# Performance work log

Hardware: AMD Instinct MI355X
Metric: run time of the kernel (lower is better)

Reference implementation:

```python
import jax, jax.numpy as jnp
import numpy as np

LMBDA = 1000.0
GAMMA = 1.0  # resolvent_gamma


def setup_inputs() -> dict:
    key = jax.random.key(0)
    k = jax.random.split(key, 6)
    B, K, N, D = 16, 128, 8000, 256
    return {
        "evals_a": jax.random.uniform(k[0], (B, K), dtype=jnp.float32) + 1e-3,
        "pinv_a": jax.random.normal(k[1], (B, K, N), dtype=jnp.float32),
        "descr_a": jax.random.normal(k[2], (B, D, N), dtype=jnp.float32),
        "evals_b": jax.random.uniform(k[3], (B, K), dtype=jnp.float32) + 1e-3,
        "pinv_b": jax.random.normal(k[4], (B, K, N), dtype=jnp.float32),
        "descr_b": jax.random.normal(k[5], (B, D, N), dtype=jnp.float32),
    }


def _compute_mask(evals_a, evals_b, gamma):
    # evals_*: [B, K]. Per-batch normalization by joint max, then resolvent mask.
    scale = jnp.maximum(evals_a.max(axis=-1), evals_b.max(axis=-1))[:, None]
    ga = jnp.power(evals_a / scale, gamma)[:, None, :]  # [B, 1, K]
    gb = jnp.power(evals_b / scale, gamma)[:, :, None]  # [B, K, 1]
    M_re = gb / (gb * gb + 1.0) - ga / (ga * ga + 1.0)
    M_im = 1.0 / (gb * gb + 1.0) - 1.0 / (ga * ga + 1.0)
    return M_re * M_re + M_im * M_im  # [B, K, K]


def _compute_fmap(sdescr_a, sdescr_b, mask, lmbda):
    # sdescr_*: [B, D, K]; mask: [B, K, K]
    AA_aa = jnp.einsum("bdk,bdl->bkl", sdescr_a, sdescr_a)  # [B, K, K]
    AA_ba = jnp.einsum("bdk,bdl->bkl", sdescr_b, sdescr_a)  # [B, K, K]
    K = mask.shape[-1]
    eye = jnp.eye(K, dtype=mask.dtype)
    # Per row i: (AA_aa + lmbda * diag(mask[b, i, :]))^{-1} AA_ba[b, i, :]^T
    A = AA_aa[:, None, :, :] + lmbda * mask[..., None] * eye  # [B, K, K, K]
    Cab = jnp.linalg.solve(A, AA_ba[..., None])[..., 0]  # [B, K, K], row i = solution
    return Cab


def reference(evals_a, pinv_a, descr_a, evals_b, pinv_b, descr_b):
    # spectral descriptor projection: (pinv @ descr^T)^T -> [B, D, K]
    sdescr_a = jnp.einsum("bkn,bdn->bdk", pinv_a, descr_a)
    sdescr_b = jnp.einsum("bkn,bdn->bdk", pinv_b, descr_b)
    mask_ab = _compute_mask(evals_a, evals_b, GAMMA)
    fmap_12 = _compute_fmap(sdescr_a, sdescr_b, mask_ab, LMBDA)
    mask_ba = _compute_mask(evals_b, evals_a, GAMMA)
    fmap_21 = _compute_fmap(sdescr_b, sdescr_a, mask_ba, LMBDA)
    return (fmap_12, fmap_21)
```

## Files before the change

### kernel.cpp

```cpp
#include <hip/hip_runtime.h>

#define BB 16
#define KD 128
#define ND 8000
#define DD 256
#define LMB 1000.0f

typedef __attribute__((ext_vector_type(8))) short bf16x8;
typedef __attribute__((ext_vector_type(4))) short bf16x4;
typedef __attribute__((ext_vector_type(4))) float f32x4;
typedef unsigned short ushort_t;

__device__ __forceinline__ void split_bf16(float x, ushort_t& h, ushort_t& l) {
    unsigned int bi = __float_as_uint(x);
    h = (ushort_t)(bi >> 16);
    float lo = x - __uint_as_float(bi & 0xFFFF0000u);
    l = (ushort_t)(__float_as_uint(lo) >> 16);
}

__device__ __forceinline__ void split_bf16_rne(float x, ushort_t& h, ushort_t& l) {
    unsigned int bi = __float_as_uint(x);
    h = (ushort_t)(bi >> 16);
    float lo = x - __uint_as_float(bi & 0xFFFF0000u);
    unsigned int lb = __float_as_uint(lo);
    lb = lb + 0x7FFFu + ((lb >> 16) & 1u);
    l = (ushort_t)(lb >> 16);
}

__device__ __forceinline__ void cvt8(f32x4 a, f32x4 b, bf16x8& h, bf16x8& l) {
    #pragma unroll
    for (int j = 0; j < 4; ++j) {
        ushort_t hh, ll;
        split_bf16(a[j], hh, ll); h[j] = (short)hh; l[j] = (short)ll;
        split_bf16(b[j], hh, ll); h[4 + j] = (short)hh; l[4 + j] = (short)ll;
    }
}

__device__ __forceinline__ void gll16(const float* g, float* l) {
    __builtin_amdgcn_global_load_lds(
        (const __attribute__((address_space(1))) void*)g,
        (__attribute__((address_space(3))) void*)l, 16, 0, 0);
}

#define ROWS 384
#define CHF 32
#define NSL 8
#define SBUF_FL 12288
#define DEPTH 3

__global__ __attribute__((amdgpu_flat_work_group_size(1024, 1024)))
void proj_kernel(
    const float* __restrict__ pinv_a, const float* __restrict__ descr_a,
    const float* __restrict__ pinv_b, const float* __restrict__ descr_b,
    float* __restrict__ sd_a, float* __restrict__ sd_b)
{
    const int b = blockIdx.x, which = blockIdx.y, s = blockIdx.z;
    const float* P  = (which ? pinv_b  : pinv_a)  + (size_t)b * KD * ND;
    const float* Dm = (which ? descr_b : descr_a) + (size_t)b * DD * ND;
    float* outp = (which ? sd_b : sd_a) + (size_t)b * KD * DD;

    __shared__ float Sbuf[DEPTH][SBUF_FL];

    const int tid = threadIdx.x;
    const int lane = tid & 63;
    const int wid = tid >> 6;
    const int wm = wid >> 2, wn = wid & 3;
    const int fr = lane & 15;
    const int kg = lane >> 4;
    const int NC = (s < 2) ? 32 : 31;

    const float* gp[3];
    int lof[3];
    #pragma unroll
    for (int u = 0; u < 3; ++u) {
        int I = wid * 3 + u;
        int r = I * 8 + (lane >> 3);
        int c4 = (lane & 7) ^ (r & 7);
        const float* rowp = (r < KD) ? (P + (size_t)r * ND) : (Dm + (size_t)(r - KD) * ND);
        gp[u] = rowp + c4 * 4;
        lof[u] = I * 256;
    }

    f32x4 acc[2][4];
    #pragma unroll
    for (int i = 0; i < 2; ++i)
        #pragma unroll
        for (int j = 0; j < 4; ++j) acc[i][j] = (f32x4){0.f, 0.f, 0.f, 0.f};

    #pragma unroll
    for (int u = 0; u < 3; ++u) gll16(gp[u] + s * CHF, &Sbuf[0][lof[u]]);
    #pragma unroll
    for (int u = 0; u < 3; ++u) gll16(gp[u] + (s + NSL) * CHF, &Sbuf[1][lof[u]]);

    for (int t = 0; t < NC; ++t) {
        if (t + 1 < NC) {
            asm volatile("s_waitcnt vmcnt(3)" ::: "memory");
        } else {
            asm volatile("s_waitcnt vmcnt(0)" ::: "memory");
        }
        __builtin_amdgcn_sched_barrier(0);
        __builtin_amdgcn_s_barrier();
        __builtin_amdgcn_sched_barrier(0);
        if (t + 2 < NC) {
            const int noff = (s + NSL * (t + 2)) * CHF;
            float* dst = &Sbuf[(t + 2) % DEPTH][0];
            #pragma unroll
            for (int u = 0; u < 3; ++u) gll16(gp[u] + noff, dst + lof[u]);
        }
        __builtin_amdgcn_sched_barrier(0);

        const float* base = &Sbuf[t % DEPTH][0];

        bf16x8 Ah[2], Al[2];
        #pragma unroll
        for (int mi = 0; mi < 2; ++mi) {
            const int rA = wm * 32 + mi * 16 + fr;
            const int ra7 = rA & 7;
            f32x4 a0 = *(const f32x4*)(base + rA * CHF + (((2 * kg)     ^ ra7) << 2));
            f32x4 a1 = *(const f32x4*)(base + rA * CHF + (((2 * kg + 1) ^ ra7) << 2));
            cvt8(a0, a1, Ah[mi], Al[mi]);
        }
        #pragma unroll
        for (int ni = 0; ni < 4; ++ni) {
            const int rB = KD + wn * 64 + ni * 16 + fr;
            const int rb7 = rB & 7;
            f32x4 b0 = *(const f32x4*)(base + rB * CHF + (((2 * kg)     ^ rb7) << 2));
            f32x4 b1 = *(const f32x4*)(base + rB * CHF + (((2 * kg + 1) ^ rb7) << 2));
            bf16x8 Bh, Bl;
            cvt8(b0, b1, Bh, Bl);
            #pragma unroll
            for (int mi = 0; mi < 2; ++mi) {
                acc[mi][ni] = __builtin_amdgcn_mfma_f32_16x16x32_bf16(Ah[mi], Bh, acc[mi][ni], 0, 0, 0);
                acc[mi][ni] = __builtin_amdgcn_mfma_f32_16x16x32_bf16(Ah[mi], Bl, acc[mi][ni], 0, 0, 0);
                acc[mi][ni] = __builtin_amdgcn_mfma_f32_16x16x32_bf16(Al[mi], Bh, acc[mi][ni], 0, 0, 0);
            }
        }
        __builtin_amdgcn_sched_barrier(0);
    }

    #pragma unroll
    for (int mi = 0; mi < 2; ++mi)
        #pragma unroll
        for (int ni = 0; ni < 4; ++ni) {
            int rbase = wm * 32 + mi * 16 + kg * 4;
            int ccol  = wn * 64 + ni * 16 + fr;
            #pragma unroll
            for (int r = 0; r < 4; ++r)
                atomicAdd(&outp[(size_t)(rbase + r) * DD + ccol], acc[mi][ni][r]);
        }
}

#define GSTR 68
__global__ __launch_bounds__(512, 2) void gram_kernel(
    const float* __restrict__ sd_a, const float* __restrict__ sd_b,
    float* __restrict__ AA)
{
    const int b = blockIdx.x, m = blockIdx.y, dchunk = blockIdx.z;
    const float* X = (m == 0) ? sd_a : sd_b;
    const float* Y = (m == 2) ? sd_a : X;
    X += (size_t)b * KD * DD;
    Y += (size_t)b * KD * DD;
    float* outp = AA + ((size_t)m * BB + b) * KD * KD;
    const int d0 = dchunk * 64;

    __shared__ ushort_t Xh[KD][GSTR], Xl[KD][GSTR];
    __shared__ ushort_t Yh[KD][GSTR], Yl[KD][GSTR];

    const int tid = threadIdx.x;
    const int lane = tid & 63;
    const int wid = tid >> 6;
    const int wm = wid >> 2, wn = wid & 3;
    const int fr = lane & 15;
    const int kg = lane >> 4;

    f32x4 acc[4][2];
    #pragma unroll
    for (int i = 0; i < 4; ++i)
        #pragma unroll
        for (int j = 0; j < 2; ++j) acc[i][j] = (f32x4){0.f, 0.f, 0.f, 0.f};

    #pragma unroll
    for (int u = 0; u < 8; ++u) {
        int idx = tid + (u & 3) * 512;
        int r = idx >> 4, c4 = idx & 15;
        const float* src = (u < 4) ? X : Y;
        float4 v = *(const float4*)(src + (size_t)r * DD + d0 + c4 * 4);
        float xs[4] = {v.x, v.y, v.z, v.w};
        bf16x4 hv, lv;
        #pragma unroll
        for (int q = 0; q < 4; ++q) {
            ushort_t hh, ll;
            split_bf16_rne(xs[q], hh, ll);
            hv[q] = (short)hh; lv[q] = (short)ll;
        }
        if (u < 4) {
            *(bf16x4*)&Xh[r][c4 * 4] = hv;
            *(bf16x4*)&Xl[r][c4 * 4] = lv;
        } else {
            *(bf16x4*)&Yh[r][c4 * 4] = hv;
            *(bf16x4*)&Yl[r][c4 * 4] = lv;
        }
    }
    __syncthreads();

    #pragma unroll
    for (int kk = 0; kk < 2; ++kk) {
        const int co = kk * 32 + kg * 8;
        bf16x8 Ah[4], Al[4];
        #pragma unroll
        for (int mi = 0; mi < 4; ++mi) {
            int r = wm * 64 + mi * 16 + fr;
            Ah[mi] = *(const bf16x8*)&Xh[r][co];
            Al[mi] = *(const bf16x8*)&Xl[r][co];
        }
        #pragma unroll
        for (int ni = 0; ni < 2; ++ni) {
            int c = wn * 32 + ni * 16 + fr;
            bf16x8 Bh = *(const bf16x8*)&Yh[c][co];
            bf16x8 Bl = *(const bf16x8*)&Yl[c][co];
            #pragma unroll
            for (int mi = 0; mi < 4; ++mi) {
                acc[mi][ni] = __builtin_amdgcn_mfma_f32_16x16x32_bf16(Ah[mi], Bh, acc[mi][ni], 0, 0, 0);
                acc[mi][ni] = __builtin_amdgcn_mfma_f32_16x16x32_bf16(Ah[mi], Bl, acc[mi][ni], 0, 0, 0);
                acc[mi][ni] = __builtin_amdgcn_mfma_f32_16x16x32_bf16(Al[mi], Bh, acc[mi][ni], 0, 0, 0);
            }
        }
    }

    #pragma unroll
    for (int mi = 0; mi < 4; ++mi)
        #pragma unroll
        for (int ni = 0; ni < 2; ++ni) {
            int rbase = wm * 64 + mi * 16 + kg * 4;
            int ccol  = wn * 32 + ni * 16 + fr;
            #pragma unroll
            for (int rr = 0; rr < 4; ++rr)
                atomicAdd(&outp[(size_t)(rbase + rr) * KD + ccol], acc[mi][ni][rr]);
        }
}

__global__ __launch_bounds__(512, 2) void invert_kernel(
    const float* __restrict__ AA, ushort_t* __restrict__ Hbf)
{
    const int b = blockIdx.x, which = blockIdx.y;
    const float* src = AA + ((size_t)which * BB + b) * KD * KD;
    ushort_t* dh = Hbf + (size_t)(which * BB + b) * 2 * KD * KD;
    ushort_t* dl = dh + (size_t)KD * KD;

    __shared__ float rowbuf[2][KD];
    __shared__ float colbuf[2][KD];

    const int tid = threadIdx.x;
    const int rb = tid >> 5;
    const int cg = tid & 31;

    f32x4 Areg[8];
    #pragma unroll
    for (int r = 0; r < 8; ++r)
        Areg[r] = *(const f32x4*)(src + (size_t)(rb * 8 + r) * KD + cg * 4);

    if (rb == 0) *(f32x4*)&rowbuf[0][cg * 4] = Areg[0];
    if (cg == 0) {
        #pragma unroll
        for (int r = 0; r < 8; ++r) colbuf[0][rb * 8 + r] = Areg[r].x;
    }
    __syncthreads();

    for (int j = 0; j < KD; ++j) {
        const int cur = j & 1, nxt = cur ^ 1;
        const int jrb = j >> 3, jr = j & 7, jcg = j >> 2, jc = j & 3;
        const float pv = 1.0f / rowbuf[cur][j];
        const f32x4 orow = *(const f32x4*)&rowbuf[cur][cg * 4];
        const f32x4 prow = orow * pv;
        const bool mycg = (cg == jcg);
        const bool myrb = (rb == jrb);

        #pragma unroll
        for (int r = 0; r < 8; ++r) {
            const float cm = colbuf[cur][rb * 8 + r];
            const float cmul = -cm * pv;
            const bool piv = myrb && (r == jr);
            f32x4 nv;
            nv.x = piv ? prow.x : fmaf(cmul, orow.x, Areg[r].x);
            nv.y = piv ? prow.y : fmaf(cmul, orow.y, Areg[r].y);
            nv.z = piv ? prow.z : fmaf(cmul, orow.z, Areg[r].z);
            nv.w = piv ? prow.w : fmaf(cmul, orow.w, Areg[r].w);
            if (mycg) {
                const float fixv = piv ? pv : cmul;
                nv.x = (jc == 0) ? fixv : nv.x;
                nv.y = (jc == 1) ? fixv : nv.y;
                nv.z = (jc == 2) ? fixv : nv.z;
                nv.w = (jc == 3) ? fixv : nv.w;
            }
            Areg[r] = nv;
        }

        if (j + 1 < KD) {
            const int njrb = (j + 1) >> 3, njr = (j + 1) & 7;
            const int njcg = (j + 1) >> 2, njc = (j + 1) & 3;
            if (rb == njrb) {
                #pragma unroll
                for (int r = 0; r < 8; ++r)
                    if (r == njr) *(f32x4*)&rowbuf[nxt][cg * 4] = Areg[r];
            }
            if (cg == njcg) {
                #pragma unroll
                for (int r = 0; r < 8; ++r) {
                    const f32x4 a = Areg[r];
                    const float e = (njc == 0) ? a.x : (njc == 1) ? a.y : (njc == 2) ? a.z : a.w;
                    colbuf[nxt][rb * 8 + r] = e;
                }
            }
        }
        __syncthreads();
    }

    #pragma unroll
    for (int r = 0; r < 8; ++r) {
        bf16x4 hv, lv;
        #pragma unroll
        for (int q = 0; q < 4; ++q) {
            ushort_t hh, ll;
            split_bf16(Areg[r][q], hh, ll);
            hv[q] = (short)hh; lv[q] = (short)ll;
        }
        const size_t off = (size_t)(rb * 8 + r) * KD + cg * 4;
        *(bf16x4*)(dh + off) = hv;
        *(bf16x4*)(dl + off) = lv;
    }
}

#define NTERMS 3
#define HSTR 136
__global__ __launch_bounds__(512) void solve_kernel(
    const float* __restrict__ AAba, const float* __restrict__ ea_g,
    const float* __restrict__ eb_g, const ushort_t* __restrict__ Hbf,
    float* __restrict__ outp)
{
    const int b = blockIdx.x, cg = blockIdx.y, which = blockIdx.z;
    const ushort_t* Hg = Hbf + (size_t)(which * BB + b) * 2 * KD * KD;
    const float* Rs = AAba + (size_t)b * KD * KD;
    float* op = outp + ((size_t)which * BB + b) * KD * KD;
    const int i0 = cg * 32;

    __shared__ ushort_t Hh[KD][HSTR], Hl[KD][HSTR];
    __shared__ ushort_t Wh[32][HSTR], Wl[32][HSTR];
    __shared__ float lmT[KD][33];
    __shared__ float tC[KD], uC[KD], tR[32], uR[32];
    __shared__ float red[256];

    const int tid = threadIdx.x;
    const int lane = tid & 63;
    const int wid = tid >> 6;
    const int wl = wid & 3, wi = wid >> 2;
    const int fr = lane & 15;
    const int kg = lane >> 4;

    if (tid < 256) {
        float e = (tid < KD) ? ea_g[b * KD + tid] : eb_g[b * KD + (tid - KD)];
        red[tid] = e;
    }
    __syncthreads();
    for (int s = 128; s > 0; s >>= 1) {
        if (tid < s) red[tid] = fmaxf(red[tid], red[tid + s]);
        __syncthreads();
    }
    const float is = 1.0f / red[0];
    const float* Ce = which ? eb_g : ea_g;
    const float* Re = which ? ea_g : eb_g;
    if (tid < KD) {
        float g = Ce[b * KD + tid] * is;
        float den = 1.0f / (g * g + 1.0f);
        tC[tid] = g * den; uC[tid] = den;
    } else if (tid < KD + 32) {
        int i = tid - KD;
        float g = Re[b * KD + i0 + i] * is;
        float den = 1.0f / (g * g + 1.0f);
        tR[i] = g * den; uR[i] = den;
    }
    __syncthreads();
    #pragma unroll
    for (int u = 0; u < 8; ++u) {
        int idx = tid + u * 512;
        int l = idx >> 5, i = idx & 31;
        float re = tR[i] - tC[l], im = uR[i] - uC[l];
        lmT[l][i] = LMB * (re * re + im * im);
    }

    #pragma unroll
    for (int u = 0; u < 4; ++u) {
        int idx = tid + u * 512;
        int row = idx >> 4, g8 = idx & 15;
        *(bf16x8*)&Hh[row][g8 * 8] = *(const bf16x8*)(Hg + (size_t)row * KD + g8 * 8);
        *(bf16x8*)&Hl[row][g8 * 8] = *(const bf16x8*)(Hg + (size_t)KD * KD + (size_t)row * KD + g8 * 8);
    }
    if (which == 0) {
        #pragma unroll
        for (int u = 0; u < 2; ++u) {
            int idx4 = (tid + u * 512) * 4;
            int i = idx4 >> 7, d = idx4 & 127;
            f32x4 v = *(const f32x4*)(Rs + (size_t)(i0 + i) * KD + d);
            bf16x4 hv, lv;
            #pragma unroll
            for (int q = 0; q < 4; ++q) {
                ushort_t hh, ll;
                split_bf16(v[q], hh, ll);
                hv[q] = (short)hh; lv[q] = (short)ll;
            }
            *(bf16x4*)&Wh[i][d] = hv;
            *(bf16x4*)&Wl[i][d] = lv;
        }
    } else {
        #pragma unroll
        for (int u = 0; u < 8; ++u) {
            int idx = tid + u * 512;
            int i = idx & 31, d = idx >> 5;
            float v = Rs[(size_t)d * KD + i0 + i];
            ushort_t hh, ll;
            split_bf16(v, hh, ll);
            Wh[i][d] = hh; Wl[i][d] = ll;
        }
    }
    __syncthreads();

    f32x4 xacc[2];
    xacc[0] = (f32x4){0.f, 0.f, 0.f, 0.f};
    xacc[1] = (f32x4){0.f, 0.f, 0.f, 0.f};

    for (int t = 0; t < NTERMS; ++t) {
        f32x4 az[2];
        az[0] = (f32x4){0.f, 0.f, 0.f, 0.f};
        az[1] = (f32x4){0.f, 0.f, 0.f, 0.f};
        #pragma unroll
        for (int kk = 0; kk < 4; ++kk) {
            const int co = kk * 32 + kg * 8;
            bf16x8 Bh = *(const bf16x8*)&Wh[wi * 16 + fr][co];
            bf16x8 Bl = *(const bf16x8*)&Wl[wi * 16 + fr][co];
            #pragma unroll
            for (int mi = 0; mi < 2; ++mi) {
                const int rA = wl * 32 + mi * 16 + fr;
                bf16x8 Ah_ = *(const bf16x8*)&Hh[rA][co];
                bf16x8 Al_ = *(const bf16x8*)&Hl[rA][co];
                az[mi] = __builtin_amdgcn_mfma_f32_16x16x32_bf16(Ah_, Bh, az[mi], 0, 0, 0);
                az[mi] = __builtin_amdgcn_mfma_f32_16x16x32_bf16(Ah_, Bl, az[mi], 0, 0, 0);
                az[mi] = __builtin_amdgcn_mfma_f32_16x16x32_bf16(Al_, Bh, az[mi], 0, 0, 0);
            }
        }
        const float sg = (t & 1) ? -1.f : 1.f;
        #pragma unroll
        for (int mi = 0; mi < 2; ++mi) {
            xacc[mi][0] += sg * az[mi][0];
            xacc[mi][1] += sg * az[mi][1];
            xacc[mi][2] += sg * az[mi][2];
            xacc[mi][3] += sg * az[mi][3];
        }
        if (t + 1 < NTERMS) {
            __syncthreads();
            const int i = wi * 16 + fr;
            #pragma unroll
            for (int mi = 0; mi < 2; ++mi) {
                const int l0 = wl * 32 + mi * 16 + kg * 4;
                bf16x4 hv, lv;
                #pragma unroll
                for (int r = 0; r < 4; ++r) {
                    float w = lmT[l0 + r][i] * az[mi][r];
                    ushort_t hh, ll;
                    split_bf16(w, hh, ll);
                    hv[r] = (short)hh; lv[r] = (short)ll;
                }
                *(bf16x4*)&Wh[i][l0] = hv;
                *(bf16x4*)&Wl[i][l0] = lv;
            }
            __syncthreads();
        }
    }

    const int i = wi * 16 + fr;
    #pragma unroll
    for (int mi = 0; mi < 2; ++mi) {
        const int l0 = wl * 32 + mi * 16 + kg * 4;
        float4 o;
        o.x = xacc[mi][0]; o.y = xacc[mi][1]; o.z = xacc[mi][2]; o.w = xacc[mi][3];
        *(float4*)(op + (size_t)(i0 + i) * KD + l0) = o;
    }
}

extern "C" void kernel_launch(void* const* d_in, const int* in_sizes, int n_in,
                              void* d_out, int out_size, void* d_ws, size_t ws_size,
                              hipStream_t stream) {
    (void)in_sizes; (void)n_in; (void)out_size; (void)ws_size;
    const float* evals_a = (const float*)d_in[0];
    const float* pinv_a  = (const float*)d_in[1];
    const float* descr_a = (const float*)d_in[2];
    const float* evals_b = (const float*)d_in[3];
    const float* pinv_b  = (const float*)d_in[4];
    const float* descr_b = (const float*)d_in[5];
    float* out = (float*)d_out;
    float* ws = (float*)d_ws;

    const size_t SD = (size_t)BB * KD * DD;
    const size_t MM = (size_t)BB * KD * KD;
    float* sd_a  = ws;
    float* sd_b  = sd_a + SD;
    float* AA    = sd_b + SD;
    ushort_t* Hbf = (ushort_t*)(AA + 3 * MM);

    hipMemsetAsync(sd_a, 0, (2 * SD + 3 * MM) * sizeof(float), stream);
    proj_kernel<<<dim3(BB, 2, NSL), 1024, 0, stream>>>(pinv_a, descr_a, pinv_b, descr_b, sd_a, sd_b);
    gram_kernel<<<dim3(BB, 3, 4), 512, 0, stream>>>(sd_a, sd_b, AA);
    invert_kernel<<<dim3(BB, 2), 512, 0, stream>>>(AA, Hbf);
    solve_kernel<<<dim3(BB, 4, 2), 512, 0, stream>>>(AA + 2 * MM, evals_a, evals_b, Hbf, out);
}
```

Baseline: 258.4 us.

## Fuse matrix inversion and Neumann-series solve into one kernel

Merges invert_kernel and solve_kernel into a single invsolve_kernel. The inverted matrix is split into bf16 hi/lo parts and written straight into shared memory rather than round-tripped through global workspace. Each block then loops over all four 32-row column groups in sequence. This removes a kernel launch and the global write and read of the inverse. In exchange, parallelism for the solve phase drops from 128 blocks to 32 blocks on a large GPU.

```diff
diff --git a/kernel.cpp b/kernel.cpp
--- a/kernel.cpp
+++ b/kernel.cpp
@@ -239,16 +239,24 @@
         }
 }
 
-__global__ __launch_bounds__(512, 2) void invert_kernel(
-    const float* __restrict__ AA, ushort_t* __restrict__ Hbf)
+#define NTERMS 3
+#define HSTR 136
+__global__ __launch_bounds__(512) void invsolve_kernel(
+    const float* __restrict__ AA, const float* __restrict__ ea_g,
+    const float* __restrict__ eb_g, float* __restrict__ outp_)
 {
     const int b = blockIdx.x, which = blockIdx.y;
     const float* src = AA + ((size_t)which * BB + b) * KD * KD;
-    ushort_t* dh = Hbf + (size_t)(which * BB + b) * 2 * KD * KD;
-    ushort_t* dl = dh + (size_t)KD * KD;
+    const float* Rs  = AA + (size_t)2 * BB * KD * KD + (size_t)b * KD * KD;
+    float* op = outp_ + ((size_t)which * BB + b) * KD * KD;
 
     __shared__ float rowbuf[2][KD];
     __shared__ float colbuf[2][KD];
+    __shared__ ushort_t Hh[KD][HSTR], Hl[KD][HSTR];
+    __shared__ ushort_t Wh[32][HSTR], Wl[32][HSTR];
+    __shared__ float lmT[KD][33];
+    __shared__ float tC[KD], uC[KD], tR[32], uR[32];
+    __shared__ float red[256];
 
     const int tid = threadIdx.x;
     const int rb = tid >> 5;
@@ -317,45 +325,14 @@
 
     #pragma unroll
     for (int r = 0; r < 8; ++r) {
-        bf16x4 hv, lv;
         #pragma unroll
         for (int q = 0; q < 4; ++q) {
             ushort_t hh, ll;
             split_bf16(Areg[r][q], hh, ll);
-            hv[q] = (short)hh; lv[q] = (short)ll;
-        }
-        const size_t off = (size_t)(rb * 8 + r) * KD + cg * 4;
-        *(bf16x4*)(dh + off) = hv;
-        *(bf16x4*)(dl + off) = lv;
-    }
-}
-
-#define NTERMS 3
-#define HSTR 136
-__global__ __launch_bounds__(512) void solve_kernel(
-    const float* __restrict__ AAba, const float* __restrict__ ea_g,
-    const float* __restrict__ eb_g, const ushort_t* __restrict__ Hbf,
-    float* __restrict__ outp)
-{
-    const int b = blockIdx.x, cg = blockIdx.y, which = blockIdx.z;
-    const ushort_t* Hg = Hbf + (size_t)(which * BB + b) * 2 * KD * KD;
-    const float* Rs = AAba + (size_t)b * KD * KD;
-    float* op = outp + ((size_t)which * BB + b) * KD * KD;
-    const int i0 = cg * 32;
-
-    __shared__ ushort_t Hh[KD][HSTR], Hl[KD][HSTR];
-    __shared__ ushort_t Wh[32][HSTR], Wl[32][HSTR];
-    __shared__ float lmT[KD][33];
-    __shared__ float tC[KD], uC[KD], tR[32], uR[32];
-    __shared__ float red[256];
-
-    const int tid = threadIdx.x;
-    const int lane = tid & 63;
-    const int wid = tid >> 6;
-    const int wl = wid & 3, wi = wid >> 2;
-    const int fr = lane & 15;
-    const int kg = lane >> 4;
-
+            Hh[rb * 8 + r][cg * 4 + q] = hh;
+            Hl[rb * 8 + r][cg * 4 + q] = ll;
+        }
+    }
     if (tid < 256) {
         float e = (tid < KD) ? ea_g[b * KD + tid] : eb_g[b * KD + (tid - KD)];
         red[tid] = e;
@@ -372,116 +349,120 @@
         float g = Ce[b * KD + tid] * is;
         float den = 1.0f / (g * g + 1.0f);
         tC[tid] = g * den; uC[tid] = den;
-    } else if (tid < KD + 32) {
-        int i = tid - KD;
-        float g = Re[b * KD + i0 + i] * is;
-        float den = 1.0f / (g * g + 1.0f);
-        tR[i] = g * den; uR[i] = den;
     }
     __syncthreads();
-    #pragma unroll
-    for (int u = 0; u < 8; ++u) {
-        int idx = tid + u * 512;
-        int l = idx >> 5, i = idx & 31;
-        float re = tR[i] - tC[l], im = uR[i] - uC[l];
-        lmT[l][i] = LMB * (re * re + im * im);
-    }
-
-    #pragma unroll
-    for (int u = 0; u < 4; ++u) {
-        int idx = tid + u * 512;
-        int row = idx >> 4, g8 = idx & 15;
-        *(bf16x8*)&Hh[row][g8 * 8] = *(const bf16x8*)(Hg + (size_t)row * KD + g8 * 8);
-        *(bf16x8*)&Hl[row][g8 * 8] = *(const bf16x8*)(Hg + (size_t)KD * KD + (size_t)row * KD + g8 * 8);
-    }
-    if (which == 0) {
-        #pragma unroll
-        for (int u = 0; u < 2; ++u) {
-            int idx4 = (tid + u * 512) * 4;
-            int i = idx4 >> 7, d = idx4 & 127;
-            f32x4 v = *(const f32x4*)(Rs + (size_t)(i0 + i) * KD + d);
-            bf16x4 hv, lv;
-            #pragma unroll
-            for (int q = 0; q < 4; ++q) {
-                ushort_t hh, ll;
-                split_bf16(v[q], hh, ll);
-                hv[q] = (short)hh; lv[q] = (short)ll;
-            }
-            *(bf16x4*)&Wh[i][d] = hv;
-            *(bf16x4*)&Wl[i][d] = lv;
-        }
-    } else {
+
+    const int lane = tid & 63;
+    const int wid = tid >> 6;
+    const int wl = wid & 3, wi = wid >> 2;
+    const int fr = lane & 15;
+    const int kg = lane >> 4;
+
+    for (int cgi = 0; cgi < 4; ++cgi) {
+        const int i0 = cgi * 32;
+        __syncthreads();
+        if (tid < 32) {
+            float g = Re[b * KD + i0 + tid] * is;
+            float den = 1.0f / (g * g + 1.0f);
+            tR[tid] = g * den; uR[tid] = den;
+        }
+        __syncthreads();
         #pragma unroll
         for (int u = 0; u < 8; ++u) {
             int idx = tid + u * 512;
-            int i = idx & 31, d = idx >> 5;
-            float v = Rs[(size_t)d * KD + i0 + i];
-            ushort_t hh, ll;
-            split_bf16(v, hh, ll);
-            Wh[i][d] = hh; Wl[i][d] = ll;
-        }
-    }
-    __syncthreads();
-
-    f32x4 xacc[2];
-    xacc[0] = (f32x4){0.f, 0.f, 0.f, 0.f};
-    xacc[1] = (f32x4){0.f, 0.f, 0.f, 0.f};
-
-    for (int t = 0; t < NTERMS; ++t) {
-        f32x4 az[2];
-        az[0] = (f32x4){0.f, 0.f, 0.f, 0.f};
-        az[1] = (f32x4){0.f, 0.f, 0.f, 0.f};
-        #pragma unroll
-        for (int kk = 0; kk < 4; ++kk) {
-            const int co = kk * 32 + kg * 8;
-            bf16x8 Bh = *(const bf16x8*)&Wh[wi * 16 + fr][co];
-            bf16x8 Bl = *(const bf16x8*)&Wl[wi * 16 + fr][co];
-            #pragma unroll
-            for (int mi = 0; mi < 2; ++mi) {
-                const int rA = wl * 32 + mi * 16 + fr;
-                bf16x8 Ah_ = *(const bf16x8*)&Hh[rA][co];
-                bf16x8 Al_ = *(const bf16x8*)&Hl[rA][co];
-                az[mi] = __builtin_amdgcn_mfma_f32_16x16x32_bf16(Ah_, Bh, az[mi], 0, 0, 0);
-                az[mi] = __builtin_amdgcn_mfma_f32_16x16x32_bf16(Ah_, Bl, az[mi], 0, 0, 0);
-                az[mi] = __builtin_amdgcn_mfma_f32_16x16x32_bf16(Al_, Bh, az[mi], 0, 0, 0);
-            }
-        }
-        const float sg = (t & 1) ? -1.f : 1.f;
-        #pragma unroll
-        for (int mi = 0; mi < 2; ++mi) {
-            xacc[mi][0] += sg * az[mi][0];
-            xacc[mi][1] += sg * az[mi][1];
-            xacc[mi][2] += sg * az[mi][2];
-            xacc[mi][3] += sg * az[mi][3];
-        }
-        if (t + 1 < NTERMS) {
-            __syncthreads();
-            const int i = wi * 16 + fr;
-            #pragma unroll
-            for (int mi = 0; mi < 2; ++mi) {
-                const int l0 = wl * 32 + mi * 16 + kg * 4;
+            int l = idx >> 5, i = idx & 31;
+            float re = tR[i] - tC[l], im = uR[i] - uC[l];
+            lmT[l][i] = LMB * (re * re + im * im);
+        }
+        if (which == 0) {
+            #pragma unroll
+            for (int u = 0; u < 2; ++u) {
+                int idx4 = (tid + u * 512) * 4;
+                int i = idx4 >> 7, d = idx4 & 127;
+                f32x4 v = *(const f32x4*)(Rs + (size_t)(i0 + i) * KD + d);
                 bf16x4 hv, lv;
                 #pragma unroll
-                for (int r = 0; r < 4; ++r) {
-                    float w = lmT[l0 + r][i] * az[mi][r];
+                for (int q = 0; q < 4; ++q) {
                     ushort_t hh, ll;
-                    split_bf16(w, hh, ll);
-                    hv[r] = (short)hh; lv[r] = (short)ll;
+                    split_bf16(v[q], hh, ll);
+                    hv[q] = (short)hh; lv[q] = (short)ll;
                 }
-                *(bf16x4*)&Wh[i][l0] = hv;
-                *(bf16x4*)&Wl[i][l0] = lv;
-            }
-            __syncthreads();
-        }
-    }
-
-    const int i = wi * 16 + fr;
-    #pragma unroll
-    for (int mi = 0; mi < 2; ++mi) {
-        const int l0 = wl * 32 + mi * 16 + kg * 4;
-        float4 o;
-        o.x = xacc[mi][0]; o.y = xacc[mi][1]; o.z = xacc[mi][2]; o.w = xacc[mi][3];
-        *(float4*)(op + (size_t)(i0 + i) * KD + l0) = o;
+                *(bf16x4*)&Wh[i][d] = hv;
+                *(bf16x4*)&Wl[i][d] = lv;
+            }
+        } else {
+            #pragma unroll
+            for (int u = 0; u < 8; ++u) {
+                int idx = tid + u * 512;
+                int i = idx & 31, d = idx >> 5;
+                float v = Rs[(size_t)d * KD + i0 + i];
+                ushort_t hh, ll;
+                split_bf16(v, hh, ll);
+                Wh[i][d] = hh; Wl[i][d] = ll;
+            }
+        }
+        __syncthreads();
+
+        f32x4 xacc[2];
+        xacc[0] = (f32x4){0.f, 0.f, 0.f, 0.f};
+        xacc[1] = (f32x4){0.f, 0.f, 0.f, 0.f};
+
+        for (int t = 0; t < NTERMS; ++t) {
+            f32x4 az[2];
+            az[0] = (f32x4){0.f, 0.f, 0.f, 0.f};
+            az[1] = (f32x4){0.f, 0.f, 0.f, 0.f};
+            #pragma unroll
+            for (int kk = 0; kk < 4; ++kk) {
+                const int co = kk * 32 + kg * 8;
+                bf16x8 Bh = *(const bf16x8*)&Wh[wi * 16 + fr][co];
+                bf16x8 Bl = *(const bf16x8*)&Wl[wi * 16 + fr][co];
+                #pragma unroll
+                for (int mi = 0; mi < 2; ++mi) {
+                    const int rA = wl * 32 + mi * 16 + fr;
+                    bf16x8 Ah_ = *(const bf16x8*)&Hh[rA][co];
+                    bf16x8 Al_ = *(const bf16x8*)&Hl[rA][co];
+                    az[mi] = __builtin_amdgcn_mfma_f32_16x16x32_bf16(Ah_, Bh, az[mi], 0, 0, 0);
+                    az[mi] = __builtin_amdgcn_mfma_f32_16x16x32_bf16(Ah_, Bl, az[mi], 0, 0, 0);
+                    az[mi] = __builtin_amdgcn_mfma_f32_16x16x32_bf16(Al_, Bh, az[mi], 0, 0, 0);
+                }
+            }
+            const float sg = (t & 1) ? -1.f : 1.f;
+            #pragma unroll
+            for (int mi = 0; mi < 2; ++mi) {
+                xacc[mi][0] += sg * az[mi][0];
+                xacc[mi][1] += sg * az[mi][1];
+                xacc[mi][2] += sg * az[mi][2];
+                xacc[mi][3] += sg * az[mi][3];
+            }
+            if (t + 1 < NTERMS) {
+                __syncthreads();
+                const int i = wi * 16 + fr;
+                #pragma unroll
+                for (int mi = 0; mi < 2; ++mi) {
+                    const int l0 = wl * 32 + mi * 16 + kg * 4;
+                    bf16x4 hv, lv;
+                    #pragma unroll
+                    for (int r = 0; r < 4; ++r) {
+                        float w = lmT[l0 + r][i] * az[mi][r];
+                        ushort_t hh, ll;
+                        split_bf16(w, hh, ll);
+                        hv[r] = (short)hh; lv[r] = (short)ll;
+                    }
+                    *(bf16x4*)&Wh[i][l0] = hv;
+                    *(bf16x4*)&Wl[i][l0] = lv;
+                }
+                __syncthreads();
+            }
+        }
+
+        const int i = wi * 16 + fr;
+        #pragma unroll
+        for (int mi = 0; mi < 2; ++mi) {
+            const int l0 = wl * 32 + mi * 16 + kg * 4;
+            float4 o;
+            o.x = xacc[mi][0]; o.y = xacc[mi][1]; o.z = xacc[mi][2]; o.w = xacc[mi][3];
+            *(float4*)(op + (size_t)(i0 + i) * KD + l0) = o;
+        }
     }
 }
 
@@ -503,11 +484,9 @@
     float* sd_a  = ws;
     float* sd_b  = sd_a + SD;
     float* AA    = sd_b + SD;
-    ushort_t* Hbf = (ushort_t*)(AA + 3 * MM);
 
     hipMemsetAsync(sd_a, 0, (2 * SD + 3 * MM) * sizeof(float), stream);
     proj_kernel<<<dim3(BB, 2, NSL), 1024, 0, stream>>>(pinv_a, descr_a, pinv_b, descr_b, sd_a, sd_b);
     gram_kernel<<<dim3(BB, 3, 4), 512, 0, stream>>>(sd_a, sd_b, AA);
-    invert_kernel<<<dim3(BB, 2), 512, 0, stream>>>(AA, Hbf);
-    solve_kernel<<<dim3(BB, 4, 2), 512, 0, stream>>>(AA + 2 * MM, evals_a, evals_b, Hbf, out);
-}
+    invsolve_kernel<<<dim3(BB, 2), 512, 0, stream>>>(AA, evals_a, evals_b, out);
+}
```

After: 273.0 us. 1.06x slower.
